# Performance work log

Measured on AMD Instinct MI355X. Metric: run time of the kernel, lower is better.

## Reference

```python
import jax, jax.numpy as jnp
import numpy as np


def setup_inputs() -> dict:
    key = jax.random.key(0)
    ks = jax.random.split(key, 8)
    B, C, P1, P2 = 8, 256, 2048, 4096
    Cq = C // 8
    return {
        "x1": jax.random.normal(ks[0], (B, C, P1), dtype=jnp.float32),
        "x2": jax.random.normal(ks[1], (B, C, P2), dtype=jnp.float32),
        "Wq": jax.random.normal(ks[2], (Cq, C), dtype=jnp.float32) * (1.0 / np.sqrt(C)),
        "bq": jnp.zeros((Cq,), dtype=jnp.float32),
        "Wk": jax.random.normal(ks[3], (Cq, C), dtype=jnp.float32) * (1.0 / np.sqrt(C)),
        "bk": jnp.zeros((Cq,), dtype=jnp.float32),
        "Wv": jax.random.normal(ks[4], (C, C), dtype=jnp.float32) * (1.0 / np.sqrt(C)),
        "bv": jnp.zeros((C,), dtype=jnp.float32),
        "alpha": jnp.ones((1,), dtype=jnp.float32),
    }


def reference(x1, x2, Wq, bq, Wk, bk, Wv, bv, alpha):
    # Conv1d(kernel_size=1) == pointwise linear over channel dim.
    # q: [B, P1, Cq]   (Q(x1) then permute(0,2,1))
    q = jnp.einsum('oc,bcp->bpo', Wq, x1) + bq[None, None, :]
    # k: [B, Cq, P2]
    k = jnp.einsum('oc,bcp->bop', Wk, x2) + bk[None, :, None]
    # v: [B, C, P1]
    v = jnp.einsum('oc,bcp->bop', Wv, x1) + bv[None, :, None]
    # energy: [B, P1, P2]; unscaled attention, softmax over P2
    energy = jnp.einsum('bpo,boq->bpq', q, k)
    attention = jax.nn.softmax(energy, axis=-1)
    # out: [B, C, P2]
    out = jnp.einsum('bcp,bpq->bcq', v, attention)
    return alpha * out + x2
```

## Files before the change

### kernel.cpp

```cpp
#include <hip/hip_runtime.h>

#define B 8
#define C 256
#define P1 2048
#define P2 4096
#define CQ 32

typedef _Float16 h8 __attribute__((ext_vector_type(8)));
typedef _Float16 h4 __attribute__((ext_vector_type(4)));
typedef float f4 __attribute__((ext_vector_type(4)));

#define MFMA16(a, b, c) __builtin_amdgcn_mfma_f32_16x16x32_f16(a, b, c, 0, 0, 0)

__global__ void prep_w(const float* __restrict__ Wq, const float* __restrict__ Wk,
                       const float* __restrict__ Wv,
                       _Float16* __restrict__ Wqh, _Float16* __restrict__ Wql,
                       _Float16* __restrict__ Wkh, _Float16* __restrict__ Wkl,
                       _Float16* __restrict__ Wvh) {
    const int i = blockIdx.x * 256 + threadIdx.x;
    if (i < CQ * C) {
        float a = Wq[i]; _Float16 h = (_Float16)a;
        Wqh[i] = h; Wql[i] = (_Float16)(a - (float)h);
        float b2 = Wk[i]; _Float16 h2 = (_Float16)b2;
        Wkh[i] = h2; Wkl[i] = (_Float16)(b2 - (float)h2);
    }
    for (int j = i; j < C * C; j += 32 * 256)
        Wvh[j] = (_Float16)Wv[j];
}

__global__ __launch_bounds__(256) void prep1(
        const float* __restrict__ x1,
        const _Float16* __restrict__ Wqh, const _Float16* __restrict__ Wql,
        const _Float16* __restrict__ Wvh,
        const float* __restrict__ bq, const float* __restrict__ bv,
        _Float16* __restrict__ qhw, _Float16* __restrict__ qlw,
        _Float16* __restrict__ vhw) {
    __shared__ float xs[32][257];
    const int t  = threadIdx.x;
    const int b  = blockIdx.x;
    const int p0 = blockIdx.y * 32;
    const float* xb = x1 + (size_t)b * C * P1;

    {
        const int pl = t & 31, cg = t >> 5;
#pragma unroll 8
        for (int i = 0; i < 32; ++i) {
            int c = cg * 32 + i;
            xs[pl][c] = xb[(size_t)c * P1 + p0 + pl];
        }
    }
    __syncthreads();

    const int w = t >> 6, lane = t & 63, ln = lane & 15, quad = lane >> 4;
    const int nh = w & 1, ch = w >> 1;
    const int prow = nh * 16 + ln;

    f4 accv[8];
#pragma unroll
    for (int mt = 0; mt < 8; ++mt) accv[mt] = (f4){0.f, 0.f, 0.f, 0.f};
    f4 accq = {0.f, 0.f, 0.f, 0.f};

    for (int ks = 0; ks < 8; ++ks) {
        const int c0 = ks * 32 + quad * 8;
        h8 bh, bl;
#pragma unroll
        for (int j = 0; j < 8; ++j) {
            float xv = xs[prow][c0 + j];
            _Float16 hh = (_Float16)xv;
            bh[j] = hh; bl[j] = (_Float16)(xv - (float)hh);
        }
#pragma unroll
        for (int mt = 0; mt < 8; ++mt) {
            h8 a = *(const h8*)&Wvh[(size_t)((ch * 8 + mt) * 16 + ln) * C + c0];
            accv[mt] = MFMA16(a, bh, accv[mt]);
            accv[mt] = MFMA16(a, bl, accv[mt]);
        }
        {
            h8 aqh = *(const h8*)&Wqh[(size_t)(ch * 16 + ln) * C + c0];
            h8 aql = *(const h8*)&Wql[(size_t)(ch * 16 + ln) * C + c0];
            accq = MFMA16(aql, bh, accq);
            accq = MFMA16(aqh, bl, accq);
            accq = MFMA16(aqh, bh, accq);
        }
    }

#pragma unroll
    for (int mt = 0; mt < 8; ++mt) {
        int cb = (ch * 8 + mt) * 16 + quad * 4;
        f4 bvv = *(const f4*)&bv[cb];
#pragma unroll
        for (int r = 0; r < 4; ++r)
            vhw[((size_t)b * C + cb + r) * P1 + p0 + prow] =
                (_Float16)(accv[mt][r] + bvv[r]);
    }
    {
        int ob = ch * 16 + quad * 4;
        f4 bqv = *(const f4*)&bq[ob];
        h4 hv, lv;
#pragma unroll
        for (int r = 0; r < 4; ++r) {
            float val = accq[r] + bqv[r];
            _Float16 hh = (_Float16)val;
            hv[r] = hh; lv[r] = (_Float16)(val - (float)hh);
        }
        size_t row = ((size_t)b * P1 + p0 + prow) * CQ + ob;
        *(h4*)(qhw + row) = hv;
        *(h4*)(qlw + row) = lv;
    }
}

__global__ __launch_bounds__(256) void prep2(
        const float* __restrict__ x2,
        const _Float16* __restrict__ Wkh, const _Float16* __restrict__ Wkl,
        const float* __restrict__ bk,
        _Float16* __restrict__ khw, _Float16* __restrict__ klw) {
    __shared__ float xs[32][257];
    const int t  = threadIdx.x;
    const int b  = blockIdx.x;
    const int p0 = blockIdx.y * 32;
    const float* xb = x2 + (size_t)b * C * P2;
    {
        const int pl = t & 31, cg = t >> 5;
#pragma unroll 8
        for (int i = 0; i < 32; ++i) {
            int c = cg * 32 + i;
            xs[pl][c] = xb[(size_t)c * P2 + p0 + pl];
        }
    }
    __syncthreads();

    const int w = t >> 6, lane = t & 63, ln = lane & 15, quad = lane >> 4;
    const int nh = w & 1, mh = w >> 1;
    const int prow = nh * 16 + ln;

    f4 accq = {0.f, 0.f, 0.f, 0.f};
    for (int ks = 0; ks < 8; ++ks) {
        const int c0 = ks * 32 + quad * 8;
        h8 bh, bl;
#pragma unroll
        for (int j = 0; j < 8; ++j) {
            float xv = xs[prow][c0 + j];
            _Float16 hh = (_Float16)xv;
            bh[j] = hh; bl[j] = (_Float16)(xv - (float)hh);
        }
        h8 akh = *(const h8*)&Wkh[(size_t)(mh * 16 + ln) * C + c0];
        h8 akl = *(const h8*)&Wkl[(size_t)(mh * 16 + ln) * C + c0];
        accq = MFMA16(akl, bh, accq);
        accq = MFMA16(akh, bl, accq);
        accq = MFMA16(akh, bh, accq);
    }
    {
        int ob = mh * 16 + quad * 4;
        f4 bkv = *(const f4*)&bk[ob];
        h4 hv, lv;
#pragma unroll
        for (int r = 0; r < 4; ++r) {
            float val = accq[r] + bkv[r];
            _Float16 hh = (_Float16)val;
            hv[r] = hh; lv[r] = (_Float16)(val - (float)hh);
        }
        size_t row = ((size_t)b * P2 + p0 + prow) * CQ + ob;
        *(h4*)(khw + row) = hv;
        *(h4*)(klw + row) = lv;
    }
}

__global__ __launch_bounds__(512) void stats_l(
        const _Float16* __restrict__ qhi, const _Float16* __restrict__ qlo,
        const _Float16* __restrict__ khi, const _Float16* __restrict__ klo,
        float* __restrict__ linv) {
    __shared__ float lred[4][32];
    const int t = threadIdx.x;
    const int b = blockIdx.x;
    const int p0 = blockIdx.y * 32;
    const int w = t >> 6, lane = t & 63, ln = lane & 15, quad = lane >> 4;
    const int ptw = w & 1, qq = w >> 1;
    const int pbase = p0 + ptw * 16;

    h8 qh = *(const h8*)(qhi + ((size_t)b * P1 + pbase + ln) * CQ + quad * 8);
    h8 ql = *(const h8*)(qlo + ((size_t)b * P1 + pbase + ln) * CQ + quad * 8);

    const _Float16* khb = khi + (size_t)b * P2 * CQ;
    const _Float16* klb = klo + (size_t)b * P2 * CQ;
    const int base = qq * 1024;

    h8 kh0 = *(const h8*)(khb + (size_t)(base + ln) * CQ + quad * 8);
    h8 kl0 = *(const h8*)(klb + (size_t)(base + ln) * CQ + quad * 8);
    h8 kh1 = *(const h8*)(khb + (size_t)(base + 16 + ln) * CQ + quad * 8);
    h8 kl1 = *(const h8*)(klb + (size_t)(base + 16 + ln) * CQ + quad * 8);

    f4 acc = {0.f, 0.f, 0.f, 0.f};
    for (int ti = 0; ti < 64; ti += 2) {
        h8 ch0 = kh0, cl0 = kl0, ch1 = kh1, cl1 = kl1;
        if (ti + 2 < 64) {
            int q2 = base + (ti + 2) * 16 + ln;
            kh0 = *(const h8*)(khb + (size_t)q2 * CQ + quad * 8);
            kl0 = *(const h8*)(klb + (size_t)q2 * CQ + quad * 8);
            kh1 = *(const h8*)(khb + (size_t)(q2 + 16) * CQ + quad * 8);
            kl1 = *(const h8*)(klb + (size_t)(q2 + 16) * CQ + quad * 8);
        }
        f4 z = {0.f, 0.f, 0.f, 0.f};
        f4 e0 = MFMA16(ql, ch0, z);
        e0 = MFMA16(qh, cl0, e0);
        e0 = MFMA16(qh, ch0, e0);
        f4 e1 = MFMA16(ql, ch1, z);
        e1 = MFMA16(qh, cl1, e1);
        e1 = MFMA16(qh, ch1, e1);
#pragma unroll
        for (int r = 0; r < 4; ++r)
            acc[r] += __expf(e0[r]) + __expf(e1[r]);
    }
#pragma unroll
    for (int off = 1; off < 16; off <<= 1) {
#pragma unroll
        for (int r = 0; r < 4; ++r) acc[r] += __shfl_xor(acc[r], off);
    }
    if (ln == 0) *(f4*)&lred[qq][ptw * 16 + quad * 4] = acc;
    __syncthreads();
    if (t < 32)
        linv[(size_t)b * P1 + p0 + t] =
            1.0f / (lred[0][t] + lred[1][t] + lred[2][t] + lred[3][t]);
}

__global__ __launch_bounds__(512, 4) void attn_gemm(
        const _Float16* __restrict__ qhi, const _Float16* __restrict__ qlo,
        const _Float16* __restrict__ khi, const _Float16* __restrict__ klo,
        const _Float16* __restrict__ vhi, const float* __restrict__ linv,
        const float* __restrict__ x2, const float* __restrict__ alpha_p,
        float* __restrict__ out) {
    __shared__ _Float16 att_s[2][64][128];

    const int t  = threadIdx.x;
    const int b  = blockIdx.x & 7;
    const int q0 = (blockIdx.x >> 3) * 64;
    const int w  = t >> 6;
    const int lane = t & 63, ln = lane & 15, quad = lane >> 4;
    const int sw = ln & 7;

    h8 kh[4], kl[4];
#pragma unroll
    for (int nt = 0; nt < 4; ++nt) {
        int q = q0 + nt * 16 + ln;
        kh[nt] = *(const h8*)(khi + ((size_t)b * P2 + q) * CQ + quad * 8);
        kl[nt] = *(const h8*)(klo + ((size_t)b * P2 + q) * CQ + quad * 8);
    }

    f4 acc[2][4];
#pragma unroll
    for (int mt = 0; mt < 2; ++mt)
#pragma unroll
        for (int nt = 0; nt < 4; ++nt) acc[mt][nt] = (f4){0.f, 0.f, 0.f, 0.f};

    h8 nqh, nql;
    {
        size_t r = ((size_t)b * P1 + w * 16 + ln) * CQ + quad * 8;
        nqh = *(const h8*)(qhi + r);
        nql = *(const h8*)(qlo + r);
    }

    const int wg   = w * 2 + (quad >> 1);
    const int wcol = ((wg ^ sw) << 3) + (quad & 1) * 4;

    for (int pc = 0; pc < P1 / 128; ++pc) {
        const int p0v = pc * 128;

        h8 av[4][2];
#pragma unroll
        for (int kk4 = 0; kk4 < 4; ++kk4)
#pragma unroll
            for (int mt = 0; mt < 2; ++mt)
                av[kk4][mt] = *(const h8*)(vhi +
                    ((size_t)b * C + w * 32 + mt * 16 + ln) * P1
                    + p0v + kk4 * 32 + quad * 8);

        h8 cqh = nqh, cql = nql;
        if (pc + 1 < P1 / 128) {
            size_t r = ((size_t)b * P1 + p0v + 128 + w * 16 + ln) * CQ + quad * 8;
            nqh = *(const h8*)(qhi + r);
            nql = *(const h8*)(qlo + r);
        }
        f4 lv = *(const f4*)(linv + (size_t)b * P1 + p0v + w * 16 + quad * 4);

        _Float16* abuf = &att_s[pc & 1][0][0];
#pragma unroll
        for (int nt = 0; nt < 4; ++nt) {
            f4 z = {0.f, 0.f, 0.f, 0.f};
            f4 e = MFMA16(cql, kh[nt], z);
            e = MFMA16(cqh, kl[nt], e);
            e = MFMA16(cqh, kh[nt], e);
            h4 pk;
#pragma unroll
            for (int r = 0; r < 4; ++r)
                pk[r] = (_Float16)(__expf(e[r]) * lv[r]);
            *(h4*)&abuf[(nt * 16 + ln) * 128 + wcol] = pk;
        }
        __syncthreads();

#pragma unroll
        for (int kk4 = 0; kk4 < 4; ++kk4) {
            h8 bf[4];
#pragma unroll
            for (int nt = 0; nt < 4; ++nt) {
                int bcol2 = kk4 * 4 + quad;
                bf[nt] = *(const h8*)&abuf[(nt * 16 + ln) * 128 + ((bcol2 ^ sw) << 3)];
            }
#pragma unroll
            for (int mt = 0; mt < 2; ++mt)
#pragma unroll
                for (int nt = 0; nt < 4; ++nt)
                    acc[mt][nt] = MFMA16(av[kk4][mt], bf[nt], acc[mt][nt]);
        }
    }

    const float alpha = alpha_p[0];
#pragma unroll
    for (int mt = 0; mt < 2; ++mt) {
#pragma unroll
        for (int nt = 0; nt < 4; ++nt) {
            int q = q0 + nt * 16 + ln;
#pragma unroll
            for (int r = 0; r < 4; ++r) {
                int c = w * 32 + mt * 16 + quad * 4 + r;
                size_t o = ((size_t)b * C + c) * P2 + q;
                out[o] = fmaf(alpha, acc[mt][nt][r], x2[o]);
            }
        }
    }
}

extern "C" void kernel_launch(void* const* d_in, const int* in_sizes, int n_in,
                              void* d_out, int out_size, void* d_ws, size_t ws_size,
                              hipStream_t stream) {
    const float* x1    = (const float*)d_in[0];
    const float* x2    = (const float*)d_in[1];
    const float* Wq    = (const float*)d_in[2];
    const float* bq    = (const float*)d_in[3];
    const float* Wk    = (const float*)d_in[4];
    const float* bk    = (const float*)d_in[5];
    const float* Wv    = (const float*)d_in[6];
    const float* bv    = (const float*)d_in[7];
    const float* alpha = (const float*)d_in[8];
    float* out = (float*)d_out;

    _Float16* qh = (_Float16*)d_ws;
    _Float16* ql = qh + (size_t)B * P1 * CQ;
    _Float16* kh = ql + (size_t)B * P1 * CQ;
    _Float16* kl = kh + (size_t)B * P2 * CQ;
    _Float16* vh = kl + (size_t)B * P2 * CQ;
    _Float16* wqh = vh + (size_t)B * C * P1;
    _Float16* wql = wqh + CQ * C;
    _Float16* wkh = wql + CQ * C;
    _Float16* wkl = wkh + CQ * C;
    _Float16* wvh = wkl + CQ * C;
    float*    li  = (float*)(wvh + C * C);

    prep_w<<<dim3(32), 256, 0, stream>>>(Wq, Wk, Wv, wqh, wql, wkh, wkl, wvh);
    prep1<<<dim3(B, P1 / 32), 256, 0, stream>>>(x1, wqh, wql, wvh, bq, bv, qh, ql, vh);
    prep2<<<dim3(B, P2 / 32), 256, 0, stream>>>(x2, wkh, wkl, bk, kh, kl);
    stats_l<<<dim3(B, P1 / 32), 512, 0, stream>>>(qh, ql, kh, kl, li);
    attn_gemm<<<dim3(512), 512, 0, stream>>>(qh, ql, kh, kl, vh, li, x2, alpha, out);
}
```

Baseline: 268.0 us.

## Double chunk size and software-pipeline V loads in attention GEMM

Grows the per-iteration P1 chunk from 128 to 256, which doubles the shared attention tile and halves the number of block barriers. V fragments are now prefetched one k-step ahead instead of all being loaded at the top of the chunk, which lowers register pressure. The Q prefetch moves after the barrier. MFMA bursts run at raised wave priority, and occupancy is pinned with waves_per_eu. The trade-off is twice the LDS per block, which may limit how many blocks fit on a CU.

```diff
diff --git a/kernel.cpp b/kernel.cpp
--- a/kernel.cpp
+++ b/kernel.cpp
@@ -222,13 +222,15 @@
             1.0f / (lred[0][t] + lred[1][t] + lred[2][t] + lred[3][t]);
 }
 
-__global__ __launch_bounds__(512, 4) void attn_gemm(
+__global__ __launch_bounds__(512)
+__attribute__((amdgpu_waves_per_eu(4, 4)))
+void attn_gemm(
         const _Float16* __restrict__ qhi, const _Float16* __restrict__ qlo,
         const _Float16* __restrict__ khi, const _Float16* __restrict__ klo,
         const _Float16* __restrict__ vhi, const float* __restrict__ linv,
         const float* __restrict__ x2, const float* __restrict__ alpha_p,
         float* __restrict__ out) {
-    __shared__ _Float16 att_s[2][64][128];
+    __shared__ _Float16 att_s[2][64][256];
 
     const int t  = threadIdx.x;
     const int b  = blockIdx.x & 7;
@@ -251,64 +253,85 @@
 #pragma unroll
         for (int nt = 0; nt < 4; ++nt) acc[mt][nt] = (f4){0.f, 0.f, 0.f, 0.f};
 
-    h8 nqh, nql;
-    {
-        size_t r = ((size_t)b * P1 + w * 16 + ln) * CQ + quad * 8;
-        nqh = *(const h8*)(qhi + r);
-        nql = *(const h8*)(qlo + r);
-    }
-
-    const int wg   = w * 2 + (quad >> 1);
-    const int wcol = ((wg ^ sw) << 3) + (quad & 1) * 4;
-
-    for (int pc = 0; pc < P1 / 128; ++pc) {
-        const int p0v = pc * 128;
-
-        h8 av[4][2];
-#pragma unroll
-        for (int kk4 = 0; kk4 < 4; ++kk4)
+    const _Float16* vrow0 = vhi + ((size_t)b * C + w * 32 + ln) * P1;
+    const _Float16* vrow1 = vrow0 + (size_t)16 * P1;
+
+    h8 avc[2];
+    avc[0] = *(const h8*)(vrow0 + quad * 8);
+    avc[1] = *(const h8*)(vrow1 + quad * 8);
+
+    h8 nqh[2], nql[2];
+#pragma unroll
+    for (int pt = 0; pt < 2; ++pt) {
+        size_t r = ((size_t)b * P1 + pt * 128 + w * 16 + ln) * CQ + quad * 8;
+        nqh[pt] = *(const h8*)(qhi + r);
+        nql[pt] = *(const h8*)(qlo + r);
+    }
+
+    for (int pc = 0; pc < P1 / 256; ++pc) {
+        const int p0v = pc * 256;
+        h8 cqh0 = nqh[0], cql0 = nql[0], cqh1 = nqh[1], cql1 = nql[1];
+
+        _Float16* abuf = &att_s[pc & 1][0][0];
+#pragma unroll
+        for (int pt = 0; pt < 2; ++pt) {
+            h8 cqh = pt ? cqh1 : cqh0;
+            h8 cql = pt ? cql1 : cql0;
+            f4 lv = *(const f4*)(linv + (size_t)b * P1 + p0v + pt * 128
+                                 + w * 16 + quad * 4);
+            const int gb = (pt << 4) + (w << 1) + (quad >> 1);
+            const int col = (((gb ^ sw) << 3)) + ((quad & 1) << 2);
+#pragma unroll
+            for (int nt = 0; nt < 4; ++nt) {
+                f4 z = {0.f, 0.f, 0.f, 0.f};
+                f4 e = MFMA16(cql, kh[nt], z);
+                e = MFMA16(cqh, kl[nt], e);
+                e = MFMA16(cqh, kh[nt], e);
+                h4 pk;
+#pragma unroll
+                for (int r = 0; r < 4; ++r)
+                    pk[r] = (_Float16)(__expf(e[r]) * lv[r]);
+                *(h4*)&abuf[(nt * 16 + ln) * 256 + col] = pk;
+            }
+        }
+        __syncthreads();
+
+        if (pc + 1 < P1 / 256) {
+#pragma unroll
+            for (int pt = 0; pt < 2; ++pt) {
+                size_t r = ((size_t)b * P1 + p0v + 256 + pt * 128
+                            + w * 16 + ln) * CQ + quad * 8;
+                nqh[pt] = *(const h8*)(qhi + r);
+                nql[pt] = *(const h8*)(qlo + r);
+            }
+        }
+
+#pragma unroll
+        for (int kk = 0; kk < 8; ++kk) {
+            h8 avn[2];
+            {
+                int pnext = p0v + (kk + 1) * 32;
+                if (pnext < P1) {
+                    avn[0] = *(const h8*)(vrow0 + pnext + quad * 8);
+                    avn[1] = *(const h8*)(vrow1 + pnext + quad * 8);
+                } else {
+                    avn[0] = avc[0]; avn[1] = avc[1];
+                }
+            }
+            h8 bf[4];
+#pragma unroll
+            for (int nt = 0; nt < 4; ++nt) {
+                int g = kk * 4 + quad;
+                bf[nt] = *(const h8*)&abuf[(nt * 16 + ln) * 256 + ((g ^ sw) << 3)];
+            }
+            __builtin_amdgcn_s_setprio(1);
 #pragma unroll
             for (int mt = 0; mt < 2; ++mt)
-                av[kk4][mt] = *(const h8*)(vhi +
-                    ((size_t)b * C + w * 32 + mt * 16 + ln) * P1
-                    + p0v + kk4 * 32 + quad * 8);
-
-        h8 cqh = nqh, cql = nql;
-        if (pc + 1 < P1 / 128) {
-            size_t r = ((size_t)b * P1 + p0v + 128 + w * 16 + ln) * CQ + quad * 8;
-            nqh = *(const h8*)(qhi + r);
-            nql = *(const h8*)(qlo + r);
-        }
-        f4 lv = *(const f4*)(linv + (size_t)b * P1 + p0v + w * 16 + quad * 4);
-
-        _Float16* abuf = &att_s[pc & 1][0][0];
-#pragma unroll
-        for (int nt = 0; nt < 4; ++nt) {
-            f4 z = {0.f, 0.f, 0.f, 0.f};
-            f4 e = MFMA16(cql, kh[nt], z);
-            e = MFMA16(cqh, kl[nt], e);
-            e = MFMA16(cqh, kh[nt], e);
-            h4 pk;
-#pragma unroll
-            for (int r = 0; r < 4; ++r)
-                pk[r] = (_Float16)(__expf(e[r]) * lv[r]);
-            *(h4*)&abuf[(nt * 16 + ln) * 128 + wcol] = pk;
-        }
-        __syncthreads();
-
-#pragma unroll
-        for (int kk4 = 0; kk4 < 4; ++kk4) {
-            h8 bf[4];
-#pragma unroll
-            for (int nt = 0; nt < 4; ++nt) {
-                int bcol2 = kk4 * 4 + quad;
-                bf[nt] = *(const h8*)&abuf[(nt * 16 + ln) * 128 + ((bcol2 ^ sw) << 3)];
-            }
-#pragma unroll
-            for (int mt = 0; mt < 2; ++mt)
 #pragma unroll
                 for (int nt = 0; nt < 4; ++nt)
-                    acc[mt][nt] = MFMA16(av[kk4][mt], bf[nt], acc[mt][nt]);
+                    acc[mt][nt] = MFMA16(avc[mt], bf[nt], acc[mt][nt]);
+            __builtin_amdgcn_s_setprio(0);
+            avc[0] = avn[0]; avc[1] = avn[1];
         }
     }
 
```

Measured after the change: 260.9 us. 1.03x faster.
